# Performance work log

Hardware: AMD Instinct MI355X
Metric: run time of the kernel (lower is better)

Reference implementation:

```python
import jax, jax.numpy as jnp
import numpy as np
from jax import lax

# dims (match init_kwargs)
NC, BS, H, W, OC, NT = 4, 16, 64, 64, 12, 32


def _conv(x, w):
    # NHWC 'same' 3x3 conv
    return lax.conv_general_dilated(x, w, (1, 1), 'SAME',
                                    dimension_numbers=('NHWC', 'HWIO', 'NHWC'))


def _convlstm_step(x, h, c, Wx, Wh, b):
    # Keras ConvLSTM2D, single timestep. Gate order i, f, g(c), o; activation=tanh,
    # recurrent_activation=hard_sigmoid.
    z = _conv(x, Wx) + _conv(h, Wh) + b
    i, f, g, o = jnp.split(z, 4, axis=-1)
    i = jax.nn.hard_sigmoid(i)
    f = jax.nn.hard_sigmoid(f)
    o = jax.nn.hard_sigmoid(o)
    c_new = f * c + i * jnp.tanh(g)
    h_new = o * jnp.tanh(c_new)
    return h_new, c_new


def setup_inputs() -> dict:
    key = jax.random.key(0)
    ks = jax.random.split(key, 8)
    sc = lambda k, shp: jax.random.normal(k, shp, jnp.float32) * 0.05
    return {
        'x': jax.random.normal(ks[0], (BS, NT, H, W, OC), jnp.float32),
        'class_ids': jax.random.randint(ks[1], (NT,), 0, NC),
        'Wx_g': sc(ks[2], (3, 3, NC * OC, 4 * OC)),  # general cell input kernel
        'Wh_g': sc(ks[3], (3, 3, OC, 4 * OC)),       # general cell recurrent kernel
        'b_g': jnp.zeros((4 * OC,), jnp.float32),
        'Wx_c': sc(ks[4], (3, 3, 2 * OC, 4 * OC)),   # class cell input kernel
        'Wh_c': sc(ks[5], (3, 3, OC, 4 * OC)),       # class cell recurrent kernel
        'b_c': jnp.zeros((4 * OC,), jnp.float32),
    }


def reference(x, class_ids, Wx_g, Wh_g, b_g, Wx_c, Wh_c, b_c):
    def step(carry, inp):
        class_h, class_c, gen_h, gen_c = carry
        frame, cid = inp
        # general cell reads the whole class-state bank (raw reshape, as in TF source)
        x_gen = jnp.reshape(class_h, (BS, H, W, NC * OC))
        gen_h, gen_c = _convlstm_step(x_gen, gen_h, gen_c, Wx_g, Wh_g, b_g)
        # class cell reads frame + fresh general representation
        aug = jnp.concatenate([frame, gen_h], axis=-1)  # (BS,H,W,2*OC)
        h_new, c_new = _convlstm_step(aug, class_h[cid], class_c[cid], Wx_c, Wh_c, b_c)
        # scatter update into class-indexed state banks
        class_h = class_h.at[cid].set(h_new)
        class_c = class_c.at[cid].set(c_new)
        return (class_h, class_c, gen_h, gen_c), h_new.reshape(BS, -1)

    z = jnp.zeros((NC, BS, H, W, OC), jnp.float32)
    g = jnp.zeros((BS, H, W, OC), jnp.float32)
    xs = (jnp.swapaxes(x, 0, 1), class_ids)  # time-major
    _, outs = lax.scan(step, (z, z, g, g), xs)
    # OuterLayer: sum over time of flattened per-step outputs
    return jnp.sum(outs, axis=0)  # (BS, H*W*OC)
```

## Files before the change

### kernel.cpp

```cpp
#include <hip/hip_runtime.h>
#include <hip/hip_bf16.h>

#define NCLS 4
#define BS   16
#define NT   32
#define OC   12
#define HW   4096
#define PIX  65536
#define STATE 786432
#define BANK  3145728

typedef short bf16x8 __attribute__((ext_vector_type(8)));
typedef float f32x4  __attribute__((ext_vector_type(4)));

__device__ __forceinline__ float hsig(float v){
    return fminf(fmaxf((v + 3.0f) * (1.0f/6.0f), 0.0f), 1.0f);
}
__device__ __forceinline__ short f2bf(float f){
    union { __hip_bfloat16 h; short s; } u;
    u.h = __float2bfloat16(f);
    return u.s;
}

__global__ __launch_bounds__(256) void repack_kernel(
    const float* __restrict__ Wxg, const float* __restrict__ Whg,
    const float* __restrict__ Wxc, const float* __restrict__ Whc,
    bf16x8* __restrict__ wgt)
{
    int id = blockIdx.x * 256 + threadIdx.x;
    if (id >= 6912) return;
    int cell = id / 3456;
    int rem  = id - cell * 3456;
    int tap  = rem / 384;  rem -= tap * 384;
    int kb   = rem / 192;  rem -= kb * 192;
    int nt   = rem / 64;
    int lane = rem - nt * 64;
    int quad = lane >> 4;
    int n    = nt * 16 + (lane & 15);
    union { bf16x8 v; short s[8]; } o;
    #pragma unroll
    for (int j = 0; j < 8; ++j){
        int k = kb * 32 + quad * 8 + j;
        float f = 0.0f;
        if (cell == 0){
            if (k < 48)      f = Wxg[(tap*48 + k)*48 + n];
            else if (k < 60) f = Whg[(tap*12 + (k-48))*48 + n];
        } else {
            if (k < 24)      f = Wxc[(tap*24 + k)*48 + n];
            else if (k < 36) f = Whc[(tap*12 + (k-24))*48 + n];
        }
        o.s[j] = f2bf(f);
    }
    wgt[id] = o.v;
}

#define HALO_SHORTS (8*198*8)

__device__ __forceinline__ int row_swizzle(int bid){
    return ((bid & 7) << 7) | (bid >> 3);
}

__global__ __launch_bounds__(256) void gen_kernel(
    short* __restrict__ bank,
    const short* __restrict__ hin,
    short* __restrict__ hout,
    float* __restrict__ cstate,
    const short* __restrict__ htmp_prev,
    const int* __restrict__ ids, int t,
    const bf16x8* __restrict__ wgt,
    const float* __restrict__ bias)
{
    __shared__ __align__(16) short halo[HALO_SHORTS];
    const int tid = threadIdx.x;
    const int rb  = row_swizzle(blockIdx.x);
    const int p0  = rb << 6;
    const int b   = p0 >> 12;
    const int y   = (p0 >> 6) & 63;

    const int cprev = (t > 0) ? ids[t-1] : -1;
    const bool slotmatch = (cprev >= 0) && ((b >> 2) == cprev);
    const short* bsrc = slotmatch ? htmp_prev : bank;

    {
        const int i = tid;
        const bool active = (i < 198);
        int r  = i / 66, c = i - r * 66;
        int yy = y + r - 1, xx = c - 1;
        bool valid = active & (yy >= 0) & (yy < 64) & (xx >= 0) & (xx < 64);
        int p  = (b << 12) + (yy << 6) + xx;
        int pb = slotmatch ? (p & 16383) : p;
        uint4 bk[6]; uint2 h0, h1, h2;
        #pragma unroll
        for (int q = 0; q < 6; ++q) bk[q] = make_uint4(0u,0u,0u,0u);
        h0 = make_uint2(0u,0u); h1 = h0; h2 = h0;
        if (valid){
            const short* bp = bsrc + pb*48;
            #pragma unroll
            for (int q = 0; q < 6; ++q) bk[q] = *(const uint4*)(bp + q*8);
            h0 = *(const uint2*)(hin + p*12);
            h1 = *(const uint2*)(hin + p*12 + 4);
            h2 = *(const uint2*)(hin + p*12 + 8);
            if (slotmatch && r == 1){
                #pragma unroll
                for (int q = 0; q < 6; ++q)
                    *(uint4*)(bank + p*48 + q*8) = bk[q];
            }
        }
        if (active){
            #pragma unroll
            for (int q = 0; q < 6; ++q)
                *(uint4*)&halo[(q*198 + i)*8] = bk[q];
            union { uint2 u2[2]; uint4 u4; } p6, p7;
            p6.u2[0] = h0; p6.u2[1] = h1;
            p7.u2[0] = h2; p7.u2[1] = make_uint2(0u,0u);
            *(uint4*)&halo[(6*198 + i)*8] = p6.u4;
            *(uint4*)&halo[(7*198 + i)*8] = p7.u4;
        }
    }
    __syncthreads();

    const int lane = tid & 63;
    const int w    = tid >> 6;
    const int m    = lane & 15;
    const int quad = lane >> 4;
    const int colbase = 16*w + m;

    f32x4 acc0 = {0.f,0.f,0.f,0.f};
    f32x4 acc1 = acc0, acc2 = acc0;
    #pragma unroll
    for (int ky = 0; ky < 3; ++ky){
        #pragma unroll
        for (int kx = 0; kx < 3; ++kx){
            const int tap = ky*3 + kx;
            #pragma unroll
            for (int kb = 0; kb < 2; ++kb){
                const bf16x8 a = *(const bf16x8*)
                    &halo[(((kb*4 + quad)*198) + ky*66 + colbase + kx)*8];
                const bf16x8* wp = wgt + ((tap*2 + kb)*3)*64 + lane;
                acc0 = __builtin_amdgcn_mfma_f32_16x16x32_bf16(a, wp[0],   acc0, 0,0,0);
                acc1 = __builtin_amdgcn_mfma_f32_16x16x32_bf16(a, wp[64],  acc1, 0,0,0);
                acc2 = __builtin_amdgcn_mfma_f32_16x16x32_bf16(a, wp[128], acc2, 0,0,0);
            }
        }
    }

    __syncthreads();
    float* zw = ((float*)halo) + w * 768;
    #pragma unroll
    for (int r = 0; r < 4; ++r){
        zw[(quad*4 + r)*48 +      m] = acc0[r];
        zw[(quad*4 + r)*48 + 16 + m] = acc1[r];
        zw[(quad*4 + r)*48 + 32 + m] = acc2[r];
    }
    __syncthreads();
    const int pbase = p0 + 16*w;
    #pragma unroll
    for (int s = 0; s < 3; ++s){
        int idx = lane*3 + s;
        int px  = idx / 12;
        int j   = idx - px*12;
        float zi = zw[px*48 +      j] + bias[j];
        float zf = zw[px*48 + 12 + j] + bias[12 + j];
        float zg = zw[px*48 + 24 + j] + bias[24 + j];
        float zo = zw[px*48 + 36 + j] + bias[36 + j];
        int off = pbase*12 + idx;
        float cold = cstate[off];
        float cn = hsig(zf)*cold + hsig(zi)*tanhf(zg);
        cstate[off] = cn;
        hout[off] = f2bf(hsig(zo)*tanhf(cn));
    }
}

__global__ __launch_bounds__(256) void class_kernel(
    const float* __restrict__ xall,
    const int*   __restrict__ ids, int t,
    const short* __restrict__ ghn,
    const short* __restrict__ bank,
    float* __restrict__ class_c,
    const bf16x8* __restrict__ wgt,
    const float* __restrict__ bias,
    short* __restrict__ htmp,
    float* __restrict__ out)
{
    __shared__ __align__(16) short halo[HALO_SHORTS];
    const int tid = threadIdx.x;
    const int rb  = row_swizzle(blockIdx.x);
    const int p0  = rb << 6;
    const int b   = p0 >> 12;
    const int y   = (p0 >> 6) & 63;
    const int cid = ids[t];
    const short* chs   = bank + (size_t)cid * STATE;
    const float* frame = xall + (size_t)(b*NT + t) * (HW*12);

    {
        const int i = tid;
        const bool active = (i < 198);
        int r  = i / 66, c = i - r * 66;
        int yy = y + r - 1, xx = c - 1;
        bool valid = active & (yy >= 0) & (yy < 64) & (xx >= 0) & (xx < 64);
        int pl = (yy << 6) + xx;
        int p  = (b << 12) + pl;
        float4 f0, f1, f2;
        f0 = make_float4(0.f,0.f,0.f,0.f); f1 = f0; f2 = f0;
        uint2 g0, g1, g2, s0, s1, s2;
        g0 = make_uint2(0u,0u); g1 = g0; g2 = g0; s0 = g0; s1 = g0; s2 = g0;
        if (valid){
            f0 = *(const float4*)(frame + pl*12);
            f1 = *(const float4*)(frame + pl*12 + 4);
            f2 = *(const float4*)(frame + pl*12 + 8);
            g0 = *(const uint2*)(ghn + p*12);
            g1 = *(const uint2*)(ghn + p*12 + 4);
            g2 = *(const uint2*)(ghn + p*12 + 8);
            s0 = *(const uint2*)(chs + p*12);
            s1 = *(const uint2*)(chs + p*12 + 4);
            s2 = *(const uint2*)(chs + p*12 + 8);
        }
        if (active){
            union { uint4 u4; uint2 u2[2]; short s[8]; } pk;
            pk.s[0]=f2bf(f0.x); pk.s[1]=f2bf(f0.y); pk.s[2]=f2bf(f0.z); pk.s[3]=f2bf(f0.w);
            pk.s[4]=f2bf(f1.x); pk.s[5]=f2bf(f1.y); pk.s[6]=f2bf(f1.z); pk.s[7]=f2bf(f1.w);
            *(uint4*)&halo[(0*198 + i)*8] = pk.u4;
            pk.s[0]=f2bf(f2.x); pk.s[1]=f2bf(f2.y); pk.s[2]=f2bf(f2.z); pk.s[3]=f2bf(f2.w);
            pk.u2[1] = g0;
            *(uint4*)&halo[(1*198 + i)*8] = pk.u4;
            pk.u2[0] = g1; pk.u2[1] = g2;
            *(uint4*)&halo[(2*198 + i)*8] = pk.u4;
            pk.u2[0] = s0; pk.u2[1] = s1;
            *(uint4*)&halo[(3*198 + i)*8] = pk.u4;
            pk.u2[0] = s2; pk.u2[1] = make_uint2(0u,0u);
            *(uint4*)&halo[(4*198 + i)*8] = pk.u4;
            uint4 z = make_uint4(0u,0u,0u,0u);
            *(uint4*)&halo[(5*198 + i)*8] = z;
            *(uint4*)&halo[(6*198 + i)*8] = z;
            *(uint4*)&halo[(7*198 + i)*8] = z;
        }
    }
    __syncthreads();

    const int lane = tid & 63;
    const int w    = tid >> 6;
    const int m    = lane & 15;
    const int quad = lane >> 4;
    const int colbase = 16*w + m;

    f32x4 acc0 = {0.f,0.f,0.f,0.f};
    f32x4 acc1 = acc0, acc2 = acc0;
    #pragma unroll
    for (int ky = 0; ky < 3; ++ky){
        #pragma unroll
        for (int kx = 0; kx < 3; ++kx){
            const int tap = ky*3 + kx;
            #pragma unroll
            for (int kb = 0; kb < 2; ++kb){
                const bf16x8 a = *(const bf16x8*)
                    &halo[(((kb*4 + quad)*198) + ky*66 + colbase + kx)*8];
                const bf16x8* wp = wgt + ((tap*2 + kb)*3)*64 + lane;
                acc0 = __builtin_amdgcn_mfma_f32_16x16x32_bf16(a, wp[0],   acc0, 0,0,0);
                acc1 = __builtin_amdgcn_mfma_f32_16x16x32_bf16(a, wp[64],  acc1, 0,0,0);
                acc2 = __builtin_amdgcn_mfma_f32_16x16x32_bf16(a, wp[128], acc2, 0,0,0);
            }
        }
    }

    __syncthreads();
    float* zw = ((float*)halo) + w * 768;
    #pragma unroll
    for (int r = 0; r < 4; ++r){
        zw[(quad*4 + r)*48 +      m] = acc0[r];
        zw[(quad*4 + r)*48 + 16 + m] = acc1[r];
        zw[(quad*4 + r)*48 + 32 + m] = acc2[r];
    }
    __syncthreads();
    float* cc = class_c + (size_t)cid * STATE;
    const int pbase = p0 + 16*w;
    #pragma unroll
    for (int s = 0; s < 3; ++s){
        int idx = lane*3 + s;
        int px  = idx / 12;
        int j   = idx - px*12;
        float zi = zw[px*48 +      j] + bias[j];
        float zf = zw[px*48 + 12 + j] + bias[12 + j];
        float zg = zw[px*48 + 24 + j] + bias[24 + j];
        float zo = zw[px*48 + 36 + j] + bias[36 + j];
        int off = pbase*12 + idx;
        float cold = cc[off];
        float cn = hsig(zf)*cold + hsig(zi)*tanhf(zg);
        cc[off] = cn;
        float h = hsig(zo)*tanhf(cn);
        htmp[off] = f2bf(h);
        out[off] += h;
    }
}

extern "C" void kernel_launch(void* const* d_in, const int* in_sizes, int n_in,
                              void* d_out, int out_size, void* d_ws, size_t ws_size,
                              hipStream_t stream)
{
    (void)in_sizes; (void)n_in; (void)out_size; (void)ws_size;
    const float* x    = (const float*)d_in[0];
    const int*   ids  = (const int*)  d_in[1];
    const float* Wxg  = (const float*)d_in[2];
    const float* Whg  = (const float*)d_in[3];
    const float* bg   = (const float*)d_in[4];
    const float* Wxc  = (const float*)d_in[5];
    const float* Whc  = (const float*)d_in[6];
    const float* bc   = (const float*)d_in[7];
    float* out = (float*)d_out;

    char* base = (char*)d_ws;
    short*  bank    = (short*) (base);
    float*  class_c = (float*) (base + 6291456);
    short*  genh0   = (short*) (base + 18874368);
    short*  genh1   = (short*) (base + 20447232);
    float*  gen_c   = (float*) (base + 22020096);
    short*  htmp0   = (short*) (base + 25165824);
    short*  htmp1   = (short*) (base + 26738688);
    bf16x8* wgt     = (bf16x8*)(base + 28311552);
    const bf16x8* wgt_gen = wgt;
    const bf16x8* wgt_cls = wgt + 3456;

    hipMemsetAsync(bank,    0, (size_t)2*BANK,  stream);
    hipMemsetAsync(class_c, 0, (size_t)4*BANK,  stream);
    hipMemsetAsync(genh0,   0, (size_t)2*STATE, stream);
    hipMemsetAsync(gen_c,   0, (size_t)4*STATE, stream);
    hipMemsetAsync(out,     0, (size_t)4*STATE, stream);

    repack_kernel<<<27, 256, 0, stream>>>(Wxg, Whg, Wxc, Whc, wgt);

    for (int t = 0; t < NT; ++t){
        short* hin       = (t & 1) ? genh1 : genh0;
        short* hnew      = (t & 1) ? genh0 : genh1;
        short* htmp_prev = (t & 1) ? htmp0 : htmp1;
        short* htmp_new  = (t & 1) ? htmp1 : htmp0;
        gen_kernel<<<1024, 256, 0, stream>>>(bank, hin, hnew, gen_c,
                                             htmp_prev, ids, t, wgt_gen, bg);
        class_kernel<<<1024, 256, 0, stream>>>(x, ids, t, hnew, bank, class_c,
                                               wgt_cls, bc, htmp_new, out);
    }
}
```

Baseline: 1.069 ms.

## Fuse general and class ConvLSTM cells into one per-step kernel with halo recompute

```diff
diff --git a/kernel.cpp b/kernel.cpp
--- a/kernel.cpp
+++ b/kernel.cpp
@@ -46,249 +46,234 @@
             if (k < 48)      f = Wxg[(tap*48 + k)*48 + n];
             else if (k < 60) f = Whg[(tap*12 + (k-48))*48 + n];
         } else {
-            if (k < 24)      f = Wxc[(tap*24 + k)*48 + n];
-            else if (k < 36) f = Whc[(tap*12 + (k-24))*48 + n];
+            if (k < 12)      f = Wxc[(tap*24 + k)*48 + n];
+            else if (k < 24) f = Whc[(tap*12 + (k-12))*48 + n];
+            else if (k < 36) f = Wxc[(tap*24 + 12 + (k-24))*48 + n];
         }
         o.s[j] = f2bf(f);
     }
     wgt[id] = o.v;
 }
 
-#define HALO_SHORTS (8*198*8)
-
-__device__ __forceinline__ int row_swizzle(int bid){
-    return ((bid & 7) << 7) | (bid >> 3);
-}
-
-__global__ __launch_bounds__(256) void gen_kernel(
+#define GH_SHORTS (8*198*8)
+#define CREG_SHORTS (6*6*66*8)
+
+__global__ __launch_bounds__(256, 1) void fused_kernel(
     short* __restrict__ bank,
     const short* __restrict__ hin,
-    short* __restrict__ hout,
-    float* __restrict__ cstate,
+    short* __restrict__ hnew,
+    const float* __restrict__ genc_in,
+    float* __restrict__ genc_out,
     const short* __restrict__ htmp_prev,
+    short* __restrict__ htmp_new,
+    const float* __restrict__ xall,
     const int* __restrict__ ids, int t,
-    const bf16x8* __restrict__ wgt,
-    const float* __restrict__ bias)
+    const bf16x8* __restrict__ wgt_gen,
+    const bf16x8* __restrict__ wgt_cls,
+    const float* __restrict__ bias_g,
+    const float* __restrict__ bias_c,
+    float* __restrict__ class_c,
+    float* __restrict__ out)
 {
-    __shared__ __align__(16) short halo[HALO_SHORTS];
-    const int tid = threadIdx.x;
-    const int rb  = row_swizzle(blockIdx.x);
-    const int p0  = rb << 6;
-    const int b   = p0 >> 12;
-    const int y   = (p0 >> 6) & 63;
-
-    const int cprev = (t > 0) ? ids[t-1] : -1;
-    const bool slotmatch = (cprev >= 0) && ((b >> 2) == cprev);
-    const short* bsrc = slotmatch ? htmp_prev : bank;
-
-    {
-        const int i = tid;
-        const bool active = (i < 198);
-        int r  = i / 66, c = i - r * 66;
-        int yy = y + r - 1, xx = c - 1;
-        bool valid = active & (yy >= 0) & (yy < 64) & (xx >= 0) & (xx < 64);
-        int p  = (b << 12) + (yy << 6) + xx;
-        int pb = slotmatch ? (p & 16383) : p;
-        uint4 bk[6]; uint2 h0, h1, h2;
-        #pragma unroll
-        for (int q = 0; q < 6; ++q) bk[q] = make_uint4(0u,0u,0u,0u);
-        h0 = make_uint2(0u,0u); h1 = h0; h2 = h0;
-        if (valid){
-            const short* bp = bsrc + pb*48;
-            #pragma unroll
-            for (int q = 0; q < 6; ++q) bk[q] = *(const uint4*)(bp + q*8);
-            h0 = *(const uint2*)(hin + p*12);
-            h1 = *(const uint2*)(hin + p*12 + 4);
-            h2 = *(const uint2*)(hin + p*12 + 8);
-            if (slotmatch && r == 1){
-                #pragma unroll
-                for (int q = 0; q < 6; ++q)
-                    *(uint4*)(bank + p*48 + q*8) = bk[q];
-            }
-        }
-        if (active){
-            #pragma unroll
-            for (int q = 0; q < 6; ++q)
-                *(uint4*)&halo[(q*198 + i)*8] = bk[q];
-            union { uint2 u2[2]; uint4 u4; } p6, p7;
-            p6.u2[0] = h0; p6.u2[1] = h1;
-            p7.u2[0] = h2; p7.u2[1] = make_uint2(0u,0u);
-            *(uint4*)&halo[(6*198 + i)*8] = p6.u4;
-            *(uint4*)&halo[(7*198 + i)*8] = p7.u4;
-        }
-    }
-    __syncthreads();
-
+    __shared__ __align__(16) short ghalo[GH_SHORTS];
+    __shared__ __align__(16) short creg[CREG_SHORTS];
+
+    const int tid  = threadIdx.x;
     const int lane = tid & 63;
     const int w    = tid >> 6;
     const int m    = lane & 15;
     const int quad = lane >> 4;
     const int colbase = 16*w + m;
 
-    f32x4 acc0 = {0.f,0.f,0.f,0.f};
-    f32x4 acc1 = acc0, acc2 = acc0;
-    #pragma unroll
-    for (int ky = 0; ky < 3; ++ky){
-        #pragma unroll
-        for (int kx = 0; kx < 3; ++kx){
-            const int tap = ky*3 + kx;
+    const int g  = ((blockIdx.x & 7) << 5) | (blockIdx.x >> 3);
+    const int b  = g >> 4;
+    const int y0 = (g & 15) * 4;
+
+    const int cid   = ids[t];
+    const int cprev = (t > 0) ? ids[t-1] : -1;
+    const bool slotmatch = (cprev >= 0) && ((b >> 2) == cprev);
+    const short* bsrc = slotmatch ? htmp_prev : bank;
+
+    for (int i = tid; i < 1188; i += 256)
+        *(uint4*)&creg[(1188 + i)*8] = make_uint4(0u,0u,0u,0u);
+
+    for (int pass = 0; pass < 6; ++pass){
+        const int yy = y0 - 1 + pass;
+        if (yy < 0 || yy > 63) continue;
+        const bool ownedrow = (pass >= 1) && (pass <= 4);
+
+        {
+            const int i = tid;
+            const bool active = (i < 198);
+            int r  = i / 66, c = i - r * 66;
+            int ry = yy + r - 1, xx = c - 1;
+            bool valid = active & (ry >= 0) & (ry < 64) & (xx >= 0) & (xx < 64);
+            int p  = (b << 12) + (ry << 6) + xx;
+            int pb = slotmatch ? (p & 16383) : p;
+            uint4 bk[6]; uint2 h0, h1, h2;
             #pragma unroll
-            for (int kb = 0; kb < 2; ++kb){
-                const bf16x8 a = *(const bf16x8*)
-                    &halo[(((kb*4 + quad)*198) + ky*66 + colbase + kx)*8];
-                const bf16x8* wp = wgt + ((tap*2 + kb)*3)*64 + lane;
-                acc0 = __builtin_amdgcn_mfma_f32_16x16x32_bf16(a, wp[0],   acc0, 0,0,0);
-                acc1 = __builtin_amdgcn_mfma_f32_16x16x32_bf16(a, wp[64],  acc1, 0,0,0);
-                acc2 = __builtin_amdgcn_mfma_f32_16x16x32_bf16(a, wp[128], acc2, 0,0,0);
-            }
-        }
-    }
-
-    __syncthreads();
-    float* zw = ((float*)halo) + w * 768;
-    #pragma unroll
-    for (int r = 0; r < 4; ++r){
-        zw[(quad*4 + r)*48 +      m] = acc0[r];
-        zw[(quad*4 + r)*48 + 16 + m] = acc1[r];
-        zw[(quad*4 + r)*48 + 32 + m] = acc2[r];
-    }
-    __syncthreads();
-    const int pbase = p0 + 16*w;
-    #pragma unroll
-    for (int s = 0; s < 3; ++s){
-        int idx = lane*3 + s;
-        int px  = idx / 12;
-        int j   = idx - px*12;
-        float zi = zw[px*48 +      j] + bias[j];
-        float zf = zw[px*48 + 12 + j] + bias[12 + j];
-        float zg = zw[px*48 + 24 + j] + bias[24 + j];
-        float zo = zw[px*48 + 36 + j] + bias[36 + j];
-        int off = pbase*12 + idx;
-        float cold = cstate[off];
-        float cn = hsig(zf)*cold + hsig(zi)*tanhf(zg);
-        cstate[off] = cn;
-        hout[off] = f2bf(hsig(zo)*tanhf(cn));
-    }
-}
-
-__global__ __launch_bounds__(256) void class_kernel(
-    const float* __restrict__ xall,
-    const int*   __restrict__ ids, int t,
-    const short* __restrict__ ghn,
-    const short* __restrict__ bank,
-    float* __restrict__ class_c,
-    const bf16x8* __restrict__ wgt,
-    const float* __restrict__ bias,
-    short* __restrict__ htmp,
-    float* __restrict__ out)
-{
-    __shared__ __align__(16) short halo[HALO_SHORTS];
-    const int tid = threadIdx.x;
-    const int rb  = row_swizzle(blockIdx.x);
-    const int p0  = rb << 6;
-    const int b   = p0 >> 12;
-    const int y   = (p0 >> 6) & 63;
-    const int cid = ids[t];
-    const short* chs   = bank + (size_t)cid * STATE;
-    const float* frame = xall + (size_t)(b*NT + t) * (HW*12);
+            for (int q = 0; q < 6; ++q) bk[q] = make_uint4(0u,0u,0u,0u);
+            h0 = make_uint2(0u,0u); h1 = h0; h2 = h0;
+            if (valid){
+                const short* bp = bsrc + pb*48;
+                #pragma unroll
+                for (int q = 0; q < 6; ++q) bk[q] = *(const uint4*)(bp + q*8);
+                h0 = *(const uint2*)(hin + p*12);
+                h1 = *(const uint2*)(hin + p*12 + 4);
+                h2 = *(const uint2*)(hin + p*12 + 8);
+                if (slotmatch && r == 1 && ownedrow){
+                    #pragma unroll
+                    for (int q = 0; q < 6; ++q)
+                        *(uint4*)(bank + p*48 + q*8) = bk[q];
+                }
+            }
+            if (active){
+                #pragma unroll
+                for (int q = 0; q < 6; ++q)
+                    *(uint4*)&ghalo[(q*198 + i)*8] = bk[q];
+                union { uint2 u2[2]; uint4 u4; } p6, p7;
+                p6.u2[0] = h0; p6.u2[1] = h1;
+                p7.u2[0] = h2; p7.u2[1] = make_uint2(0u,0u);
+                *(uint4*)&ghalo[(6*198 + i)*8] = p6.u4;
+                *(uint4*)&ghalo[(7*198 + i)*8] = p7.u4;
+            }
+        }
+        __syncthreads();
+
+        f32x4 acc0 = {0.f,0.f,0.f,0.f};
+        f32x4 acc1 = acc0, acc2 = acc0;
+        #pragma unroll
+        for (int ky = 0; ky < 3; ++ky){
+            #pragma unroll
+            for (int kx = 0; kx < 3; ++kx){
+                const int tap = ky*3 + kx;
+                #pragma unroll
+                for (int kb = 0; kb < 2; ++kb){
+                    const bf16x8 a = *(const bf16x8*)
+                        &ghalo[(((kb*4 + quad)*198) + ky*66 + colbase + kx)*8];
+                    const bf16x8* wp = wgt_gen + ((tap*2 + kb)*3)*64 + lane;
+                    acc0 = __builtin_amdgcn_mfma_f32_16x16x32_bf16(a, wp[0],   acc0, 0,0,0);
+                    acc1 = __builtin_amdgcn_mfma_f32_16x16x32_bf16(a, wp[64],  acc1, 0,0,0);
+                    acc2 = __builtin_amdgcn_mfma_f32_16x16x32_bf16(a, wp[128], acc2, 0,0,0);
+                }
+            }
+        }
+        __syncthreads();
+
+        float* zw = ((float*)ghalo) + w * 768;
+        #pragma unroll
+        for (int r2 = 0; r2 < 4; ++r2){
+            zw[(quad*4 + r2)*48 +      m] = acc0[r2];
+            zw[(quad*4 + r2)*48 + 16 + m] = acc1[r2];
+            zw[(quad*4 + r2)*48 + 32 + m] = acc2[r2];
+        }
+        const int pbase = (b << 12) + (yy << 6) + 16*w;
+        #pragma unroll
+        for (int s = 0; s < 3; ++s){
+            int idx = lane*3 + s;
+            int px  = idx / 12;
+            int j   = idx - px*12;
+            float zi = zw[px*48 +      j] + bias_g[j];
+            float zf = zw[px*48 + 12 + j] + bias_g[12 + j];
+            float zg = zw[px*48 + 24 + j] + bias_g[24 + j];
+            float zo = zw[px*48 + 36 + j] + bias_g[36 + j];
+            int off = pbase*12 + idx;
+            float cn = hsig(zf)*genc_in[off] + hsig(zi)*tanhf(zg);
+            float h  = hsig(zo)*tanhf(cn);
+            short hb = f2bf(h);
+            if (ownedrow){
+                genc_out[off] = cn;
+                hnew[off] = hb;
+            }
+            int plane = 3 + (j >> 3), slot = j & 7, hcol = px + 16*w + 1;
+            creg[((plane*6 + pass)*66 + hcol)*8 + slot] = hb;
+        }
+        __syncthreads();
+    }
 
     {
-        const int i = tid;
-        const bool active = (i < 198);
-        int r  = i / 66, c = i - r * 66;
-        int yy = y + r - 1, xx = c - 1;
-        bool valid = active & (yy >= 0) & (yy < 64) & (xx >= 0) & (xx < 64);
-        int pl = (yy << 6) + xx;
-        int p  = (b << 12) + pl;
-        float4 f0, f1, f2;
-        f0 = make_float4(0.f,0.f,0.f,0.f); f1 = f0; f2 = f0;
-        uint2 g0, g1, g2, s0, s1, s2;
-        g0 = make_uint2(0u,0u); g1 = g0; g2 = g0; s0 = g0; s1 = g0; s2 = g0;
-        if (valid){
-            f0 = *(const float4*)(frame + pl*12);
-            f1 = *(const float4*)(frame + pl*12 + 4);
-            f2 = *(const float4*)(frame + pl*12 + 8);
-            g0 = *(const uint2*)(ghn + p*12);
-            g1 = *(const uint2*)(ghn + p*12 + 4);
-            g2 = *(const uint2*)(ghn + p*12 + 8);
-            s0 = *(const uint2*)(chs + p*12);
-            s1 = *(const uint2*)(chs + p*12 + 4);
-            s2 = *(const uint2*)(chs + p*12 + 8);
-        }
-        if (active){
-            union { uint4 u4; uint2 u2[2]; short s[8]; } pk;
+        const short* chs = (cid == cprev) ? htmp_prev
+                                          : (bank + (size_t)cid * STATE);
+        const float* frame = xall + (size_t)(b*NT + t) * (HW*12);
+        for (int i = tid; i < 396; i += 256){
+            int hr = i / 66, c = i - hr*66;
+            int ry = y0 - 1 + hr, xx = c - 1;
+            bool valid = (ry >= 0) & (ry < 64) & (xx >= 0) & (xx < 64);
+            int pl = (ry << 6) + xx;
+            int p  = (b << 12) + pl;
+            float4 f0 = make_float4(0.f,0.f,0.f,0.f), f1 = f0, f2 = f0;
+            uint2 u0 = make_uint2(0u,0u), u1 = u0, u2 = u0;
+            if (valid){
+                f0 = *(const float4*)(frame + pl*12);
+                f1 = *(const float4*)(frame + pl*12 + 4);
+                f2 = *(const float4*)(frame + pl*12 + 8);
+                u0 = *(const uint2*)(chs + p*12);
+                u1 = *(const uint2*)(chs + p*12 + 4);
+                u2 = *(const uint2*)(chs + p*12 + 8);
+            }
+            union { uint4 u4; uint2 u2s[2]; short s[8]; } pk;
             pk.s[0]=f2bf(f0.x); pk.s[1]=f2bf(f0.y); pk.s[2]=f2bf(f0.z); pk.s[3]=f2bf(f0.w);
             pk.s[4]=f2bf(f1.x); pk.s[5]=f2bf(f1.y); pk.s[6]=f2bf(f1.z); pk.s[7]=f2bf(f1.w);
-            *(uint4*)&halo[(0*198 + i)*8] = pk.u4;
+            *(uint4*)&creg[((0*6 + hr)*66 + c)*8] = pk.u4;
             pk.s[0]=f2bf(f2.x); pk.s[1]=f2bf(f2.y); pk.s[2]=f2bf(f2.z); pk.s[3]=f2bf(f2.w);
-            pk.u2[1] = g0;
-            *(uint4*)&halo[(1*198 + i)*8] = pk.u4;
-            pk.u2[0] = g1; pk.u2[1] = g2;
-            *(uint4*)&halo[(2*198 + i)*8] = pk.u4;
-            pk.u2[0] = s0; pk.u2[1] = s1;
-            *(uint4*)&halo[(3*198 + i)*8] = pk.u4;
-            pk.u2[0] = s2; pk.u2[1] = make_uint2(0u,0u);
-            *(uint4*)&halo[(4*198 + i)*8] = pk.u4;
-            uint4 z = make_uint4(0u,0u,0u,0u);
-            *(uint4*)&halo[(5*198 + i)*8] = z;
-            *(uint4*)&halo[(6*198 + i)*8] = z;
-            *(uint4*)&halo[(7*198 + i)*8] = z;
+            pk.u2s[1] = u0;
+            *(uint4*)&creg[((1*6 + hr)*66 + c)*8] = pk.u4;
+            pk.u2s[0] = u1; pk.u2s[1] = u2;
+            *(uint4*)&creg[((2*6 + hr)*66 + c)*8] = pk.u4;
         }
     }
     __syncthreads();
 
-    const int lane = tid & 63;
-    const int w    = tid >> 6;
-    const int m    = lane & 15;
-    const int quad = lane >> 4;
-    const int colbase = 16*w + m;
-
-    f32x4 acc0 = {0.f,0.f,0.f,0.f};
-    f32x4 acc1 = acc0, acc2 = acc0;
-    #pragma unroll
-    for (int ky = 0; ky < 3; ++ky){
-        #pragma unroll
-        for (int kx = 0; kx < 3; ++kx){
-            const int tap = ky*3 + kx;
+    float* cc = class_c + (size_t)cid * STATE;
+    const int kb1plane = (quad == 0) ? 4 : 5;
+    for (int rr = 0; rr < 4; ++rr){
+        f32x4 acc0 = {0.f,0.f,0.f,0.f};
+        f32x4 acc1 = acc0, acc2 = acc0;
+        #pragma unroll
+        for (int ky = 0; ky < 3; ++ky){
             #pragma unroll
-            for (int kb = 0; kb < 2; ++kb){
-                const bf16x8 a = *(const bf16x8*)
-                    &halo[(((kb*4 + quad)*198) + ky*66 + colbase + kx)*8];
-                const bf16x8* wp = wgt + ((tap*2 + kb)*3)*64 + lane;
-                acc0 = __builtin_amdgcn_mfma_f32_16x16x32_bf16(a, wp[0],   acc0, 0,0,0);
-                acc1 = __builtin_amdgcn_mfma_f32_16x16x32_bf16(a, wp[64],  acc1, 0,0,0);
-                acc2 = __builtin_amdgcn_mfma_f32_16x16x32_bf16(a, wp[128], acc2, 0,0,0);
-            }
-        }
-    }
-
-    __syncthreads();
-    float* zw = ((float*)halo) + w * 768;
-    #pragma unroll
-    for (int r = 0; r < 4; ++r){
-        zw[(quad*4 + r)*48 +      m] = acc0[r];
-        zw[(quad*4 + r)*48 + 16 + m] = acc1[r];
-        zw[(quad*4 + r)*48 + 32 + m] = acc2[r];
-    }
-    __syncthreads();
-    float* cc = class_c + (size_t)cid * STATE;
-    const int pbase = p0 + 16*w;
-    #pragma unroll
-    for (int s = 0; s < 3; ++s){
-        int idx = lane*3 + s;
-        int px  = idx / 12;
-        int j   = idx - px*12;
-        float zi = zw[px*48 +      j] + bias[j];
-        float zf = zw[px*48 + 12 + j] + bias[12 + j];
-        float zg = zw[px*48 + 24 + j] + bias[24 + j];
-        float zo = zw[px*48 + 36 + j] + bias[36 + j];
-        int off = pbase*12 + idx;
-        float cold = cc[off];
-        float cn = hsig(zf)*cold + hsig(zi)*tanhf(zg);
-        cc[off] = cn;
-        float h = hsig(zo)*tanhf(cn);
-        htmp[off] = f2bf(h);
-        out[off] += h;
+            for (int kx = 0; kx < 3; ++kx){
+                const int tap = ky*3 + kx;
+                const int hr  = rr + ky;
+                const bf16x8 a0 = *(const bf16x8*)
+                    &creg[((quad*6 + hr)*66 + colbase + kx)*8];
+                const bf16x8* wp0 = wgt_cls + ((tap*2 + 0)*3)*64 + lane;
+                acc0 = __builtin_amdgcn_mfma_f32_16x16x32_bf16(a0, wp0[0],   acc0, 0,0,0);
+                acc1 = __builtin_amdgcn_mfma_f32_16x16x32_bf16(a0, wp0[64],  acc1, 0,0,0);
+                acc2 = __builtin_amdgcn_mfma_f32_16x16x32_bf16(a0, wp0[128], acc2, 0,0,0);
+                const bf16x8 a1 = *(const bf16x8*)
+                    &creg[((kb1plane*6 + hr)*66 + colbase + kx)*8];
+                const bf16x8* wp1 = wgt_cls + ((tap*2 + 1)*3)*64 + lane;
+                acc0 = __builtin_amdgcn_mfma_f32_16x16x32_bf16(a1, wp1[0],   acc0, 0,0,0);
+                acc1 = __builtin_amdgcn_mfma_f32_16x16x32_bf16(a1, wp1[64],  acc1, 0,0,0);
+                acc2 = __builtin_amdgcn_mfma_f32_16x16x32_bf16(a1, wp1[128], acc2, 0,0,0);
+            }
+        }
+        float* zw = ((float*)ghalo) + w * 768;
+        #pragma unroll
+        for (int r2 = 0; r2 < 4; ++r2){
+            zw[(quad*4 + r2)*48 +      m] = acc0[r2];
+            zw[(quad*4 + r2)*48 + 16 + m] = acc1[r2];
+            zw[(quad*4 + r2)*48 + 32 + m] = acc2[r2];
+        }
+        const int pbase = (b << 12) + ((y0 + rr) << 6) + 16*w;
+        #pragma unroll
+        for (int s = 0; s < 3; ++s){
+            int idx = lane*3 + s;
+            int px  = idx / 12;
+            int j   = idx - px*12;
+            float zi = zw[px*48 +      j] + bias_c[j];
+            float zf = zw[px*48 + 12 + j] + bias_c[12 + j];
+            float zg = zw[px*48 + 24 + j] + bias_c[24 + j];
+            float zo = zw[px*48 + 36 + j] + bias_c[36 + j];
+            int off = pbase*12 + idx;
+            float cn = hsig(zf)*cc[off] + hsig(zi)*tanhf(zg);
+            cc[off] = cn;
+            float h = hsig(zo)*tanhf(cn);
+            htmp_new[off] = f2bf(h);
+            out[off] += h;
+        }
+        __syncthreads();
     }
 }
 
@@ -309,32 +294,31 @@
 
     char* base = (char*)d_ws;
     short*  bank    = (short*) (base);
-    float*  class_c = (float*) (base + 6291456);
-    short*  genh0   = (short*) (base + 18874368);
-    short*  genh1   = (short*) (base + 20447232);
-    float*  gen_c   = (float*) (base + 22020096);
-    short*  htmp0   = (short*) (base + 25165824);
-    short*  htmp1   = (short*) (base + 26738688);
-    bf16x8* wgt     = (bf16x8*)(base + 28311552);
+    float*  class_c = (float*) (base +  6291456);
+    float*  genc0   = (float*) (base + 18874368);
+    short*  genh0   = (short*) (base + 22020096);
+    float*  genc1   = (float*) (base + 23592960);
+    short*  genh1   = (short*) (base + 26738688);
+    short*  htmp0   = (short*) (base + 28311552);
+    short*  htmp1   = (short*) (base + 29884416);
+    bf16x8* wgt     = (bf16x8*)(base + 31457280);
     const bf16x8* wgt_gen = wgt;
     const bf16x8* wgt_cls = wgt + 3456;
 
-    hipMemsetAsync(bank,    0, (size_t)2*BANK,  stream);
-    hipMemsetAsync(class_c, 0, (size_t)4*BANK,  stream);
-    hipMemsetAsync(genh0,   0, (size_t)2*STATE, stream);
-    hipMemsetAsync(gen_c,   0, (size_t)4*STATE, stream);
-    hipMemsetAsync(out,     0, (size_t)4*STATE, stream);
+    hipMemsetAsync(base, 0, (size_t)23592960, stream);
+    hipMemsetAsync(out,  0, (size_t)4*STATE,  stream);
 
     repack_kernel<<<27, 256, 0, stream>>>(Wxg, Whg, Wxc, Whc, wgt);
 
     for (int t = 0; t < NT; ++t){
-        short* hin       = (t & 1) ? genh1 : genh0;
-        short* hnew      = (t & 1) ? genh0 : genh1;
-        short* htmp_prev = (t & 1) ? htmp0 : htmp1;
-        short* htmp_new  = (t & 1) ? htmp1 : htmp0;
-        gen_kernel<<<1024, 256, 0, stream>>>(bank, hin, hnew, gen_c,
-                                             htmp_prev, ids, t, wgt_gen, bg);
-        class_kernel<<<1024, 256, 0, stream>>>(x, ids, t, hnew, bank, class_c,
-                                               wgt_cls, bc, htmp_new, out);
-    }
-}
+        const short* hi = (t & 1) ? genh1 : genh0;
+        short*       hn = (t & 1) ? genh0 : genh1;
+        const float* gi = (t & 1) ? genc1 : genc0;
+        float*       go = (t & 1) ? genc0 : genc1;
+        const short* hp = (t & 1) ? htmp0 : htmp1;
+        short*       hw2= (t & 1) ? htmp1 : htmp0;
+        fused_kernel<<<256, 256, 0, stream>>>(bank, hi, hn, gi, go, hp, hw2,
+                                              x, ids, t, wgt_gen, wgt_cls,
+                                              bg, bc, class_c, out);
+    }
+}
```

Result: slower. 1.179 ms (+10.3%).
